# Optimization experiments

Hardware: AMD Instinct MI355X
Metric: run time of the kernel (lower is better)

## Reference

```python
import jax, jax.numpy as jnp
import numpy as np
from jax import lax

B, T, H, NCLS = 512, 2048, 64, 10


def _lstm_layer(x_seq, w_ih, w_hh, b_ih, b_hh):
    """x_seq: [B, T, I]. Returns (outputs [B, T, H], last hidden [B, H]).
    PyTorch gate order: i, f, g, o."""
    Bn = x_seq.shape[0]
    Hn = w_hh.shape[1]
    # Precompute input projections for all timesteps: [T, B, 4H]
    gx = jnp.einsum('bti,gi->tbg', x_seq, w_ih) + (b_ih + b_hh)

    def step(carry, gx_t):
        h, c = carry
        g = gx_t + h @ w_hh.T  # [B, 4H]
        i, f, gg, o = jnp.split(g, 4, axis=-1)
        i = jax.nn.sigmoid(i)
        f = jax.nn.sigmoid(f)
        gg = jnp.tanh(gg)
        o = jax.nn.sigmoid(o)
        c = f * c + i * gg
        h = o * jnp.tanh(c)
        return (h, c), h

    h0 = jnp.zeros((Bn, Hn), x_seq.dtype)
    (h_last, _), hs = lax.scan(step, (h0, h0), gx)
    return jnp.swapaxes(hs, 0, 1), h_last


def setup_inputs() -> dict:
    key = jax.random.key(0)
    ks = jax.random.split(key, 16)
    s = 1.0 / np.sqrt(H)
    u = lambda k, shape: jax.random.uniform(k, shape, jnp.float32, -s, s)
    inp = {
        'x': jax.random.normal(ks[0], (B, T), jnp.float32),
        # LSTM layer 0 (input size 1)
        'w_ih0': u(ks[1], (4 * H, 1)),
        'w_hh0': u(ks[2], (4 * H, H)),
        'b_ih0': u(ks[3], (4 * H,)),
        'b_hh0': u(ks[4], (4 * H,)),
        # LSTM layer 1 (input size H)
        'w_ih1': u(ks[5], (4 * H, H)),
        'w_hh1': u(ks[6], (4 * H, H)),
        'b_ih1': u(ks[7], (4 * H,)),
        'b_hh1': u(ks[8], (4 * H,)),
        # classifier head: 64 -> 64 -> 32 -> NCLS
        'w1': jax.random.normal(ks[9], (64, H), jnp.float32) * s,
        'b1': jnp.zeros((64,), jnp.float32),
        'w2': jax.random.normal(ks[10], (32, 64), jnp.float32) * (1.0 / np.sqrt(64)),
        'b2': jnp.zeros((32,), jnp.float32),
        'w3': jax.random.normal(ks[11], (NCLS, 32), jnp.float32) * (1.0 / np.sqrt(32)),
        'b3': jnp.zeros((NCLS,), jnp.float32),
    }
    return inp


def reference(x, w_ih0, w_hh0, b_ih0, b_hh0, w_ih1, w_hh1, b_ih1, b_hh1,
              w1, b1, w2, b2, w3, b3):
    # x: [B, T] -> [B, T, 1]
    xs = x[..., None]
    out0, _ = _lstm_layer(xs, w_ih0, w_hh0, b_ih0, b_hh0)
    # dropout(0.2) between LSTM layers is inactive in eval mode
    _, h_last = _lstm_layer(out0, w_ih1, w_hh1, b_ih1, b_hh1)
    # classifier (dropouts inactive in eval)
    h = jax.nn.relu(h_last @ w1.T + b1)
    h = jax.nn.relu(h @ w2.T + b2)
    return h @ w3.T + b3
```

## Files before the change

kernel.cpp:

```cpp
#include <hip/hip_runtime.h>
#include <math.h>

#define TT 2048
#define HH 64
#define NE 4
#define NBLK 128
#define NTHR 512

typedef _Float16 half8 __attribute__((ext_vector_type(8)));
typedef float f32x4 __attribute__((ext_vector_type(4)));

__device__ __forceinline__ float sigmoid_fast(float x) {
    float e = __expf(-x);
    return __builtin_amdgcn_rcpf(1.0f + e);
}
__device__ __forceinline__ float tanh_fast(float x) {
    float e = __expf(-2.0f * x);
    return fmaf(2.0f, __builtin_amdgcn_rcpf(1.0f + e), -1.0f);
}
__device__ __forceinline__ float sel4(f32x4 v, int r) {
    float s01 = (r & 1) ? v[1] : v[0];
    float s23 = (r & 1) ? v[3] : v[2];
    return (r & 2) ? s23 : s01;
}

__global__ __launch_bounds__(NTHR) __attribute__((amdgpu_waves_per_eu(4, 4)))
void lstm_direct_kernel(const float* __restrict__ x,
                        const float* __restrict__ w_ih0,
                        const float* __restrict__ w_hh0,
                        const float* __restrict__ b_ih0,
                        const float* __restrict__ b_hh0,
                        const float* __restrict__ w_ih1,
                        const float* __restrict__ w_hh1,
                        const float* __restrict__ b_ih1,
                        const float* __restrict__ b_hh1,
                        const float* __restrict__ w1, const float* __restrict__ b1,
                        const float* __restrict__ w2, const float* __restrict__ b2,
                        const float* __restrict__ w3, const float* __restrict__ b3,
                        float* __restrict__ out)
{
    const int tid = threadIdx.x;
    const int wv  = tid >> 6;
    const int l   = tid & 63;
    const int L   = wv >> 2;
    const int j   = wv & 3;
    const int e16 = l & 15;
    const int kg  = l >> 4;
    const int bA  = blockIdx.x * NE;

    __shared__ __align__(16) float xs[(TT + 1) * (NE + 1)];
    __shared__ __align__(16) _Float16 hsw[2][2][16 * 64];
    __shared__ float cls1[NE][HH];
    __shared__ float cls2[NE][32];

    for (int i = tid; i < 2 * 2 * 16 * 64; i += NTHR)
        ((_Float16*)hsw)[i] = (_Float16)0.0f;
    for (int i = tid; i < NE * TT; i += NTHR) {
        const int e = i >> 11, t = i & (TT - 1);
        xs[t * (NE + 1) + e] = x[(size_t)(bA + e) * TT + t];
    }
    if (tid < NE + 1) xs[TT * (NE + 1) + tid] = 0.0f;

    half8 wf[16];
    {
        auto frag = [&](const float* M, int g, int kc) {
            const int row = g * 64 + 16 * j + e16;
            half8 v;
            #pragma unroll
            for (int i = 0; i < 8; ++i) v[i] = (_Float16)M[row * HH + kc * 32 + kg * 8 + i];
            return v;
        };
        const float* M01 = L ? w_ih1 : w_hh0;
        #pragma unroll
        for (int g = 0; g < 4; ++g) {
            wf[4 * g + 0] = frag(M01, g, 0);
            wf[4 * g + 1] = frag(M01, g, 1);
            if (L) {
                wf[4 * g + 2] = frag(w_hh1, g, 0);
                wf[4 * g + 3] = frag(w_hh1, g, 1);
            } else {
                half8 zz;
                #pragma unroll
                for (int i = 0; i < 8; ++i) zz[i] = (_Float16)0.0f;
                wf[4 * g + 2] = zz;
                wf[4 * g + 3] = zz;
            }
        }
    }

    const int rsel = e16 >> 2;
    const int au = 16 * j + 4 * kg + rsel;
    const int ae = e16 & 3;
    float bi[4], wxr[4];
    {
        const float* bihp = L ? b_ih1 : b_ih0;
        const float* bhhp = L ? b_hh1 : b_hh0;
        #pragma unroll
        for (int g = 0; g < 4; ++g) {
            bi[g]  = bihp[g * 64 + au] + bhhp[g * 64 + au];
            wxr[g] = L ? 0.0f : w_ih0[g * 64 + au];
        }
    }
    #pragma unroll
    for (int i = 0; i < 16; ++i) asm volatile("" : "+v"(wf[i]));
    #pragma unroll
    for (int g = 0; g < 4; ++g) {
        asm volatile("" : "+v"(bi[g]));
        asm volatile("" : "+v"(wxr[g]));
    }

    float c = 0.0f;

    const int swz4 = (ae & 7) << 4;
    const int hro0 = ae * 128 + ((16 * kg) ^ swz4);
    const int hro1 = ae * 128 + ((64 + 16 * kg) ^ swz4);
    const int hwb  = ae * 128 + ((2 * au) ^ (ae << 4));
    const f32x4 z4 = {0.0f, 0.0f, 0.0f, 0.0f};

    __syncthreads();

    for (int t = 0; t <= TT; ++t) {
        const int rp = t & 1;
        f32x4 acc[4];
        if (L) {
            const char* h0r = (const char*)&hsw[0][rp][0];
            const char* h1r = (const char*)&hsw[1][rp][0];
            half8 f0 = *(const half8*)(h0r + hro0);
            half8 f1 = *(const half8*)(h0r + hro1);
            half8 f2 = *(const half8*)(h1r + hro0);
            half8 f3 = *(const half8*)(h1r + hro1);
            #pragma unroll
            for (int g = 0; g < 4; ++g) {
                acc[g] = __builtin_amdgcn_mfma_f32_16x16x32_f16(wf[4 * g + 0], f0, z4, 0, 0, 0);
                acc[g] = __builtin_amdgcn_mfma_f32_16x16x32_f16(wf[4 * g + 1], f1, acc[g], 0, 0, 0);
                acc[g] = __builtin_amdgcn_mfma_f32_16x16x32_f16(wf[4 * g + 2], f2, acc[g], 0, 0, 0);
                acc[g] = __builtin_amdgcn_mfma_f32_16x16x32_f16(wf[4 * g + 3], f3, acc[g], 0, 0, 0);
            }
        } else {
            const char* h0r = (const char*)&hsw[0][rp][0];
            half8 f0 = *(const half8*)(h0r + hro0);
            half8 f1 = *(const half8*)(h0r + hro1);
            #pragma unroll
            for (int g = 0; g < 4; ++g) {
                acc[g] = __builtin_amdgcn_mfma_f32_16x16x32_f16(wf[4 * g + 0], f0, z4, 0, 0, 0);
                acc[g] = __builtin_amdgcn_mfma_f32_16x16x32_f16(wf[4 * g + 1], f1, acc[g], 0, 0, 0);
            }
        }
        {
            float z0 = sel4(acc[0], rsel);
            float z1 = sel4(acc[1], rsel);
            float z2 = sel4(acc[2], rsel);
            float z3 = sel4(acc[3], rsel);
            const float xt = xs[t * (NE + 1) + ae];
            z0 += fmaf(wxr[0], xt, bi[0]);
            z1 += fmaf(wxr[1], xt, bi[1]);
            z2 += fmaf(wxr[2], xt, bi[2]);
            z3 += fmaf(wxr[3], xt, bi[3]);
            float gi = sigmoid_fast(z0);
            float gf = sigmoid_fast(z1);
            float gg = tanh_fast(z2);
            float go = sigmoid_fast(z3);
            c = fmaf(gf, c, gi * gg);
            float h = go * tanh_fast(c);
            if (L && t == 0) { c = 0.0f; h = 0.0f; }
            *(_Float16*)((char*)&hsw[L][rp ^ 1][0] + hwb) = (_Float16)h;
        }
        __syncthreads();
    }

    if (wv < 4) {
        const char* h1f = (const char*)&hsw[1][1][0];
        float a = b1[l];
        #pragma unroll 8
        for (int k = 0; k < HH; ++k) {
            const float hk = (float)*(const _Float16*)(h1f + wv * 128 + ((2 * k) ^ (wv << 4)));
            a = fmaf(w1[l * HH + k], hk, a);
        }
        cls1[wv][l] = fmaxf(a, 0.0f);
    }
    __syncthreads();
    if (wv < 4 && l < 32) {
        float a = b2[l];
        #pragma unroll 8
        for (int k = 0; k < HH; ++k) a = fmaf(w2[l * HH + k], cls1[wv][k], a);
        cls2[wv][l] = fmaxf(a, 0.0f);
    }
    __syncthreads();
    if (wv < 4 && l < 10) {
        float a = b3[l];
        #pragma unroll
        for (int k = 0; k < 32; ++k) a = fmaf(w3[l * 32 + k], cls2[wv][k], a);
        out[(size_t)(bA + wv) * 10 + l] = a;
    }
}

extern "C" void kernel_launch(void* const* d_in, const int* in_sizes, int n_in,
                              void* d_out, int out_size, void* d_ws, size_t ws_size,
                              hipStream_t stream) {
    const float* x     = (const float*)d_in[0];
    const float* w_ih0 = (const float*)d_in[1];
    const float* w_hh0 = (const float*)d_in[2];
    const float* b_ih0 = (const float*)d_in[3];
    const float* b_hh0 = (const float*)d_in[4];
    const float* w_ih1 = (const float*)d_in[5];
    const float* w_hh1 = (const float*)d_in[6];
    const float* b_ih1 = (const float*)d_in[7];
    const float* b_hh1 = (const float*)d_in[8];
    const float* w1    = (const float*)d_in[9];
    const float* b1    = (const float*)d_in[10];
    const float* w2    = (const float*)d_in[11];
    const float* b2    = (const float*)d_in[12];
    const float* w3    = (const float*)d_in[13];
    const float* b3    = (const float*)d_in[14];
    float* out = (float*)d_out;

    lstm_direct_kernel<<<NBLK, NTHR, 0, stream>>>(x, w_ih0, w_hh0, b_ih0, b_hh0,
                                                  w_ih1, w_hh1, b_ih1, b_hh1,
                                                  w1, b1, w2, b2, w3, b3, out);
}
```

Measured before the change: 856.6 us.

## Merge both LSTM layers into symmetric four-wave blocks with two sequences each

Each wave now computes gates for both LSTM layers at once, holding fragments of w_hh0, w_ih1 and w_hh1, and lanes pick layer 0 or layer 1 results by lane index. Blocks shrink to 4 waves handling 2 sequences each, so the grid doubles to 256 blocks and the per-step barrier spans fewer waves. The intent is to spread the recurrence over more CUs, removing the layer-0 and layer-1 wave imbalance and making barriers cheaper. In exchange each wave issues 24 MFMAs per step instead of 8 or 16, and half of every 16-column MFMA output is unused because only 2 of 4 sequence columns are live.

```diff
diff --git a/kernel.cpp b/kernel.cpp
--- a/kernel.cpp
+++ b/kernel.cpp
@@ -3,9 +3,9 @@
 
 #define TT 2048
 #define HH 64
-#define NE 4
-#define NBLK 128
-#define NTHR 512
+#define NE 2
+#define NBLK 256
+#define NTHR 256
 
 typedef _Float16 half8 __attribute__((ext_vector_type(8)));
 typedef float f32x4 __attribute__((ext_vector_type(4)));
@@ -24,26 +24,25 @@
     return (r & 2) ? s23 : s01;
 }
 
-__global__ __launch_bounds__(NTHR) __attribute__((amdgpu_waves_per_eu(4, 4)))
-void lstm_direct_kernel(const float* __restrict__ x,
-                        const float* __restrict__ w_ih0,
-                        const float* __restrict__ w_hh0,
-                        const float* __restrict__ b_ih0,
-                        const float* __restrict__ b_hh0,
-                        const float* __restrict__ w_ih1,
-                        const float* __restrict__ w_hh1,
-                        const float* __restrict__ b_ih1,
-                        const float* __restrict__ b_hh1,
-                        const float* __restrict__ w1, const float* __restrict__ b1,
-                        const float* __restrict__ w2, const float* __restrict__ b2,
-                        const float* __restrict__ w3, const float* __restrict__ b3,
-                        float* __restrict__ out)
+__global__ __launch_bounds__(NTHR) __attribute__((amdgpu_waves_per_eu(1, 1)))
+void lstm_sym4_kernel(const float* __restrict__ x,
+                      const float* __restrict__ w_ih0,
+                      const float* __restrict__ w_hh0,
+                      const float* __restrict__ b_ih0,
+                      const float* __restrict__ b_hh0,
+                      const float* __restrict__ w_ih1,
+                      const float* __restrict__ w_hh1,
+                      const float* __restrict__ b_ih1,
+                      const float* __restrict__ b_hh1,
+                      const float* __restrict__ w1, const float* __restrict__ b1,
+                      const float* __restrict__ w2, const float* __restrict__ b2,
+                      const float* __restrict__ w3, const float* __restrict__ b3,
+                      float* __restrict__ out)
 {
     const int tid = threadIdx.x;
     const int wv  = tid >> 6;
     const int l   = tid & 63;
-    const int L   = wv >> 2;
-    const int j   = wv & 3;
+    const int j   = wv;
     const int e16 = l & 15;
     const int kg  = l >> 4;
     const int bA  = blockIdx.x * NE;
@@ -61,7 +60,7 @@
     }
     if (tid < NE + 1) xs[TT * (NE + 1) + tid] = 0.0f;
 
-    half8 wf[16];
+    half8 w0f[8], wif[8], whf[8];
     {
         auto frag = [&](const float* M, int g, int kc) {
             const int row = g * 64 + 16 * j + e16;
@@ -70,39 +69,37 @@
             for (int i = 0; i < 8; ++i) v[i] = (_Float16)M[row * HH + kc * 32 + kg * 8 + i];
             return v;
         };
-        const float* M01 = L ? w_ih1 : w_hh0;
         #pragma unroll
         for (int g = 0; g < 4; ++g) {
-            wf[4 * g + 0] = frag(M01, g, 0);
-            wf[4 * g + 1] = frag(M01, g, 1);
-            if (L) {
-                wf[4 * g + 2] = frag(w_hh1, g, 0);
-                wf[4 * g + 3] = frag(w_hh1, g, 1);
-            } else {
-                half8 zz;
-                #pragma unroll
-                for (int i = 0; i < 8; ++i) zz[i] = (_Float16)0.0f;
-                wf[4 * g + 2] = zz;
-                wf[4 * g + 3] = zz;
-            }
-        }
-    }
-
-    const int rsel = e16 >> 2;
-    const int au = 16 * j + 4 * kg + rsel;
-    const int ae = e16 & 3;
+            w0f[2 * g + 0] = frag(w_hh0, g, 0);
+            w0f[2 * g + 1] = frag(w_hh0, g, 1);
+            wif[2 * g + 0] = frag(w_ih1, g, 0);
+            wif[2 * g + 1] = frag(w_ih1, g, 1);
+            whf[2 * g + 0] = frag(w_hh1, g, 0);
+            whf[2 * g + 1] = frag(w_hh1, g, 1);
+        }
+    }
+
+    const int Lsel = e16 >> 3;
+    const int rsel = (e16 >> 1) & 3;
+    const int ae   = e16 & 1;
+    const int au   = 16 * j + 4 * kg + rsel;
     float bi[4], wxr[4];
     {
-        const float* bihp = L ? b_ih1 : b_ih0;
-        const float* bhhp = L ? b_hh1 : b_hh0;
+        const float* bihp = Lsel ? b_ih1 : b_ih0;
+        const float* bhhp = Lsel ? b_hh1 : b_hh0;
         #pragma unroll
         for (int g = 0; g < 4; ++g) {
             bi[g]  = bihp[g * 64 + au] + bhhp[g * 64 + au];
-            wxr[g] = L ? 0.0f : w_ih0[g * 64 + au];
+            wxr[g] = Lsel ? 0.0f : w_ih0[g * 64 + au];
         }
     }
     #pragma unroll
-    for (int i = 0; i < 16; ++i) asm volatile("" : "+v"(wf[i]));
+    for (int i = 0; i < 8; ++i) {
+        asm volatile("" : "+v"(w0f[i]));
+        asm volatile("" : "+v"(wif[i]));
+        asm volatile("" : "+v"(whf[i]));
+    }
     #pragma unroll
     for (int g = 0; g < 4; ++g) {
         asm volatile("" : "+v"(bi[g]));
@@ -111,46 +108,37 @@
 
     float c = 0.0f;
 
-    const int swz4 = (ae & 7) << 4;
-    const int hro0 = ae * 128 + ((16 * kg) ^ swz4);
-    const int hro1 = ae * 128 + ((64 + 16 * kg) ^ swz4);
-    const int hwb  = ae * 128 + ((2 * au) ^ (ae << 4));
+    const int swz  = ae << 4;
+    const int hro0 = ae * 128 + ((16 * kg) ^ swz);
+    const int hro1 = ae * 128 + ((64 + 16 * kg) ^ swz);
+    const int hwb  = ae * 128 + ((2 * au) ^ swz);
     const f32x4 z4 = {0.0f, 0.0f, 0.0f, 0.0f};
 
     __syncthreads();
 
     for (int t = 0; t <= TT; ++t) {
         const int rp = t & 1;
-        f32x4 acc[4];
-        if (L) {
-            const char* h0r = (const char*)&hsw[0][rp][0];
-            const char* h1r = (const char*)&hsw[1][rp][0];
-            half8 f0 = *(const half8*)(h0r + hro0);
-            half8 f1 = *(const half8*)(h0r + hro1);
-            half8 f2 = *(const half8*)(h1r + hro0);
-            half8 f3 = *(const half8*)(h1r + hro1);
-            #pragma unroll
-            for (int g = 0; g < 4; ++g) {
-                acc[g] = __builtin_amdgcn_mfma_f32_16x16x32_f16(wf[4 * g + 0], f0, z4, 0, 0, 0);
-                acc[g] = __builtin_amdgcn_mfma_f32_16x16x32_f16(wf[4 * g + 1], f1, acc[g], 0, 0, 0);
-                acc[g] = __builtin_amdgcn_mfma_f32_16x16x32_f16(wf[4 * g + 2], f2, acc[g], 0, 0, 0);
-                acc[g] = __builtin_amdgcn_mfma_f32_16x16x32_f16(wf[4 * g + 3], f3, acc[g], 0, 0, 0);
-            }
-        } else {
-            const char* h0r = (const char*)&hsw[0][rp][0];
-            half8 f0 = *(const half8*)(h0r + hro0);
-            half8 f1 = *(const half8*)(h0r + hro1);
-            #pragma unroll
-            for (int g = 0; g < 4; ++g) {
-                acc[g] = __builtin_amdgcn_mfma_f32_16x16x32_f16(wf[4 * g + 0], f0, z4, 0, 0, 0);
-                acc[g] = __builtin_amdgcn_mfma_f32_16x16x32_f16(wf[4 * g + 1], f1, acc[g], 0, 0, 0);
-            }
+        const char* h0r = (const char*)&hsw[0][rp][0];
+        const char* h1r = (const char*)&hsw[1][rp][0];
+        half8 f0 = *(const half8*)(h0r + hro0);
+        half8 f1 = *(const half8*)(h0r + hro1);
+        half8 f2 = *(const half8*)(h1r + hro0);
+        half8 f3 = *(const half8*)(h1r + hro1);
+        f32x4 a0[4], a1[4];
+        #pragma unroll
+        for (int g = 0; g < 4; ++g) {
+            a0[g] = __builtin_amdgcn_mfma_f32_16x16x32_f16(w0f[2 * g + 0], f0, z4, 0, 0, 0);
+            a1[g] = __builtin_amdgcn_mfma_f32_16x16x32_f16(wif[2 * g + 0], f0, z4, 0, 0, 0);
+            a0[g] = __builtin_amdgcn_mfma_f32_16x16x32_f16(w0f[2 * g + 1], f1, a0[g], 0, 0, 0);
+            a1[g] = __builtin_amdgcn_mfma_f32_16x16x32_f16(wif[2 * g + 1], f1, a1[g], 0, 0, 0);
+            a1[g] = __builtin_amdgcn_mfma_f32_16x16x32_f16(whf[2 * g + 0], f2, a1[g], 0, 0, 0);
+            a1[g] = __builtin_amdgcn_mfma_f32_16x16x32_f16(whf[2 * g + 1], f3, a1[g], 0, 0, 0);
         }
         {
-            float z0 = sel4(acc[0], rsel);
-            float z1 = sel4(acc[1], rsel);
-            float z2 = sel4(acc[2], rsel);
-            float z3 = sel4(acc[3], rsel);
+            float z0 = Lsel ? sel4(a1[0], rsel) : sel4(a0[0], rsel);
+            float z1 = Lsel ? sel4(a1[1], rsel) : sel4(a0[1], rsel);
+            float z2 = Lsel ? sel4(a1[2], rsel) : sel4(a0[2], rsel);
+            float z3 = Lsel ? sel4(a1[3], rsel) : sel4(a0[3], rsel);
             const float xt = xs[t * (NE + 1) + ae];
             z0 += fmaf(wxr[0], xt, bi[0]);
             z1 += fmaf(wxr[1], xt, bi[1]);
@@ -162,13 +150,13 @@
             float go = sigmoid_fast(z3);
             c = fmaf(gf, c, gi * gg);
             float h = go * tanh_fast(c);
-            if (L && t == 0) { c = 0.0f; h = 0.0f; }
-            *(_Float16*)((char*)&hsw[L][rp ^ 1][0] + hwb) = (_Float16)h;
+            if (Lsel && t == 0) { c = 0.0f; h = 0.0f; }
+            *(_Float16*)((char*)&hsw[Lsel][rp ^ 1][0] + hwb) = (_Float16)h;
         }
         __syncthreads();
     }
 
-    if (wv < 4) {
+    if (wv < NE) {
         const char* h1f = (const char*)&hsw[1][1][0];
         float a = b1[l];
         #pragma unroll 8
@@ -179,14 +167,14 @@
         cls1[wv][l] = fmaxf(a, 0.0f);
     }
     __syncthreads();
-    if (wv < 4 && l < 32) {
+    if (wv < NE && l < 32) {
         float a = b2[l];
         #pragma unroll 8
         for (int k = 0; k < HH; ++k) a = fmaf(w2[l * HH + k], cls1[wv][k], a);
         cls2[wv][l] = fmaxf(a, 0.0f);
     }
     __syncthreads();
-    if (wv < 4 && l < 10) {
+    if (wv < NE && l < 10) {
         float a = b3[l];
         #pragma unroll
         for (int k = 0; k < 32; ++k) a = fmaf(w3[l * 32 + k], cls2[wv][k], a);
@@ -214,7 +202,7 @@
     const float* b3    = (const float*)d_in[14];
     float* out = (float*)d_out;
 
-    lstm_direct_kernel<<<NBLK, NTHR, 0, stream>>>(x, w_ih0, w_hh0, b_ih0, b_hh0,
-                                                  w_ih1, w_hh1, b_ih1, b_hh1,
-                                                  w1, b1, w2, b2, w3, b3, out);
-}
+    lstm_sym4_kernel<<<NBLK, NTHR, 0, stream>>>(x, w_ih0, w_hh0, b_ih0, b_hh0,
+                                                w_ih1, w_hh1, b_ih1, b_hh1,
+                                                w1, b1, w2, b2, w3, b3, out);
+}
```

New measurement: 1.011 ms. +18.0%, slower.
